# Kernel optimization log

Hardware: AMD Instinct MI355X
Metric: run time of the kernel (lower is better)

Reference implementation:

```python
import jax, jax.numpy as jnp
import numpy as np

# norse default LIF/LI parameters
DT = 0.001
TAU_SYN_INV = 200.0
TAU_MEM_INV = 100.0
V_TH = 1.0
ALPHA = 100.0        # SuperSpike surrogate slope (method='super', alpha=100)
T_ENC = 40           # ConstantCurrentLIFEncoder(40)
SCALE = 50.0

STATE_DIM = 256
ACTIONS = 18
HIDDEN = 128
BATCH = 1024

@jax.custom_vjp
def spike(x):
    return (x > 0).astype(x.dtype)

def _spike_fwd(x):
    return spike(x), x

def _spike_bwd(x, g):
    # SuperSpike surrogate: 1 / (alpha*|x| + 1)^2
    return (g / (ALPHA * jnp.abs(x) + 1.0) ** 2,)

spike.defvjp(_spike_fwd, _spike_bwd)

def encode(current):
    # constant-current LIF encoder: current [B, D] -> spikes [T_ENC, B, D]
    def step(v, _):
        v = v + DT * TAU_MEM_INV * (-v + current)   # v_leak = 0
        z = spike(v - V_TH)
        v = (1.0 - z) * v                            # reset to v_reset = 0
        return v, z
    _, zs = jax.lax.scan(step, jnp.zeros_like(current), None, length=T_ENC)
    return zs

def snn_forward(x, w_in, w_rec, w_actor, w_critic):
    # encode positive and negative rectified currents, concat on feature dim
    xs = jnp.concatenate([encode(jax.nn.relu(SCALE * x)),
                          encode(jax.nn.relu(-SCALE * x))], axis=2)  # [T, B, 2D]
    B = x.shape[0]
    H = w_in.shape[0]
    A = w_actor.shape[0]
    dt_ = x.dtype
    carry0 = (jnp.zeros((B, H), dt_), jnp.zeros((B, H), dt_), jnp.zeros((B, H), dt_),
              jnp.zeros((B, A), dt_), jnp.zeros((B, A), dt_),
              jnp.zeros((B, 1), dt_), jnp.zeros((B, 1), dt_))

    def step(carry, x_t):
        z, v, i, va, ia, vc, ic = carry
        # --- recurrent LIFCell (norse lif_step) ---
        v_dec = v + DT * TAU_MEM_INV * (-v + i)      # dv uses pre-decay i
        i_dec = i - DT * TAU_SYN_INV * i
        z_new = spike(v_dec - V_TH)
        v_new = (1.0 - z_new) * v_dec                # reset by z to v_reset = 0
        i_new = i_dec + x_t @ w_in.T + z @ w_rec.T   # recurrent input uses old z
        # --- LICell actor readout (norse li_step) ---
        va_new = va + DT * TAU_MEM_INV * (-va + ia)
        ia_new = ia - DT * TAU_SYN_INV * ia + z_new @ w_actor.T
        # --- LICell critic readout ---
        vc_new = vc + DT * TAU_MEM_INV * (-vc + ic)
        ic_new = ic - DT * TAU_SYN_INV * ic + z_new @ w_critic.T
        return (z_new, v_new, i_new, va_new, ia_new, vc_new, ic_new), (va_new, vc_new)

    _, (volt_a, volt_c) = jax.lax.scan(step, carry0, xs)
    m_a = jnp.max(volt_a, axis=0)                    # max over time
    m_c = jnp.max(volt_c, axis=0)
    return jax.nn.softmax(m_a, axis=1), m_c


def setup_inputs() -> dict:
    key = jax.random.key(0)
    k0, k1, k2, k3, k4 = jax.random.split(key, 5)
    in_feat = 2 * STATE_DIM
    x = jax.random.normal(k0, (BATCH, STATE_DIM), dtype=jnp.float32)
    # norse init: randn * sqrt(2 / input_size)
    w_in = jax.random.normal(k1, (HIDDEN, in_feat), dtype=jnp.float32) * np.sqrt(2.0 / in_feat)
    w_rec = jax.random.normal(k2, (HIDDEN, HIDDEN), dtype=jnp.float32) * np.sqrt(2.0 / HIDDEN)
    w_actor = jax.random.normal(k3, (ACTIONS, HIDDEN), dtype=jnp.float32) * np.sqrt(2.0 / HIDDEN)
    w_critic = jax.random.normal(k4, (1, HIDDEN), dtype=jnp.float32) * np.sqrt(2.0 / HIDDEN)
    return {"x": x, "w_in": w_in, "w_rec": w_rec, "w_actor": w_actor, "w_critic": w_critic}


def reference(x, w_in, w_rec, w_actor, w_critic):
    return snn_forward(x, w_in, w_rec, w_actor, w_critic)
```

## Files before the change

### kernel.cpp

```cpp
#include <hip/hip_runtime.h>
#include <hip/hip_bf16.h>
#include <stdint.h>

typedef __attribute__((ext_vector_type(4))) float f32x4;
typedef __attribute__((ext_vector_type(8))) short s16x8;
typedef __attribute__((ext_vector_type(4))) unsigned int u32x4;

#define OFF_I 2621440

__device__ __forceinline__ void lut_entry(uint32_t by, uint32_t* r) {
    uint32_t r0 = 0, r1 = 0, r2 = 0, r3 = 0;
    if (by & 1)   r0 |= 0x3F80u;
    if (by & 2)   r0 |= 0x3F800000u;
    if (by & 4)   r1 |= 0x3F80u;
    if (by & 8)   r1 |= 0x3F800000u;
    if (by & 16)  r2 |= 0x3F80u;
    if (by & 32)  r2 |= 0x3F800000u;
    if (by & 64)  r3 |= 0x3F80u;
    if (by & 128) r3 |= 0x3F800000u;
    r[0] = r0; r[1] = r1; r[2] = r2; r[3] = r3;
}

__global__ __launch_bounds__(256) void k_encode(const float* __restrict__ x,
                                                uint32_t* __restrict__ spk) {
    int gid  = blockIdx.x * 256 + threadIdx.x;
    int b    = gid >> 9;
    int f    = gid & 511;
    int lane = threadIdx.x & 63;
    float xv  = x[b * 256 + (f & 255)];
    float cur = (f < 256) ? fmaxf(50.f * xv, 0.f) : fmaxf(-50.f * xv, 0.f);
    int wbase = (f >> 6) << 1;
    float v = 0.f;
    for (int t = 0; t < 40; ++t) {
        v = v + 0.1f * (cur - v);
        bool z = (v - 1.0f) > 0.f;
        unsigned long long m = __ballot(z);
        if (z) v = 0.f;
        if (lane == 0)
            *(unsigned long long*)&spk[(size_t)(t * 1024 + b) * 16 + wbase] = m;
    }
}

__global__ __launch_bounds__(512, 1) void k_ingemm(const uint32_t* __restrict__ spk,
                                                   const float* __restrict__ w_in,
                                                   float* __restrict__ I) {
    __shared__ uint32_t lut[256][4];
    __shared__ float tile[16][128];
    const int tid = threadIdx.x;
    if (tid < 256) lut_entry(tid, lut[tid]);
    const int lane = tid & 63, wid = tid >> 6;
    const int fr = lane & 15, fo = lane >> 4;
    const int n0 = wid * 16;

#define LOADB(i) s16x8 bh##i, bl##i; { \
    const float* p = w_in + (n0 + fr) * 512 + (i) * 32 + fo * 8; \
    f32x4 fa = *(const f32x4*)p; f32x4 fb = *(const f32x4*)(p + 4); \
    _Pragma("unroll") for (int j = 0; j < 8; ++j) { \
        float f = (j < 4) ? fa[j] : fb[j - 4]; \
        __hip_bfloat16 hb = __float2bfloat16(f); \
        float r1 = f - __bfloat162float(hb); \
        __hip_bfloat16 lb = __float2bfloat16(r1); \
        bh##i[j] = (short)*(unsigned short*)&hb; \
        bl##i[j] = (short)*(unsigned short*)&lb; } }
    LOADB(0)  LOADB(1)  LOADB(2)  LOADB(3)  LOADB(4)  LOADB(5)  LOADB(6)  LOADB(7)
    LOADB(8)  LOADB(9)  LOADB(10) LOADB(11) LOADB(12) LOADB(13) LOADB(14) LOADB(15)
#undef LOADB
    asm volatile("" : "+v"(bh0), "+v"(bh1), "+v"(bh2),  "+v"(bh3),
                      "+v"(bh4), "+v"(bh5), "+v"(bh6),  "+v"(bh7),
                      "+v"(bh8), "+v"(bh9), "+v"(bh10), "+v"(bh11),
                      "+v"(bh12),"+v"(bh13),"+v"(bh14), "+v"(bh15));
    asm volatile("" : "+v"(bl0), "+v"(bl1), "+v"(bl2),  "+v"(bl3),
                      "+v"(bl4), "+v"(bl5), "+v"(bl6),  "+v"(bl7),
                      "+v"(bl8), "+v"(bl9), "+v"(bl10), "+v"(bl11),
                      "+v"(bl12),"+v"(bl13),"+v"(bl14), "+v"(bl15));
    __syncthreads();

    const int m0 = blockIdx.x * 160;
    const int srow = tid >> 5;
    const int sc0  = (tid & 31) * 4;
    for (int mt = 0; mt < 10; ++mt) {
        int mrow = m0 + mt * 16 + fr;
        u32x4 w0 = *(const u32x4*)&spk[mrow * 16];
        u32x4 w1 = *(const u32x4*)&spk[mrow * 16 + 4];
        u32x4 w2 = *(const u32x4*)&spk[mrow * 16 + 8];
        u32x4 w3 = *(const u32x4*)&spk[mrow * 16 + 12];
        f32x4 acc = (f32x4)0.f;
#define KSTEP(i, WSEL) { uint32_t by = ((WSEL) >> (fo * 8)) & 0xFFu; \
        union { u32x4 u; s16x8 v; } cv; cv.u = *(const u32x4*)lut[by]; \
        acc = __builtin_amdgcn_mfma_f32_16x16x32_bf16(cv.v, bh##i, acc, 0, 0, 0); \
        acc = __builtin_amdgcn_mfma_f32_16x16x32_bf16(cv.v, bl##i, acc, 0, 0, 0); }
        KSTEP(0,  w0[0]) KSTEP(1,  w0[1]) KSTEP(2,  w0[2]) KSTEP(3,  w0[3])
        KSTEP(4,  w1[0]) KSTEP(5,  w1[1]) KSTEP(6,  w1[2]) KSTEP(7,  w1[3])
        KSTEP(8,  w2[0]) KSTEP(9,  w2[1]) KSTEP(10, w2[2]) KSTEP(11, w2[3])
        KSTEP(12, w3[0]) KSTEP(13, w3[1]) KSTEP(14, w3[2]) KSTEP(15, w3[3])
#undef KSTEP
        __syncthreads();
#pragma unroll
        for (int r = 0; r < 4; ++r)
            tile[fo * 4 + r][n0 + fr] = acc[r];
        __syncthreads();
        f32x4 vv = *(const f32x4*)&tile[srow][sc0];
        *(f32x4*)&I[(size_t)(m0 + mt * 16 + srow) * 128 + sc0] = vv;
    }
}

__global__ __launch_bounds__(512, 1) void k_recur_ro(const float* __restrict__ I,
                                                     const float* __restrict__ w_rec,
                                                     const float* __restrict__ w_actor,
                                                     const float* __restrict__ w_critic,
                                                     float* __restrict__ out) {
    __shared__ uint32_t lut[256][4];
    __shared__ __align__(16) uint16_t zm16[2][16][8];
    __shared__ float smax[16][20];
    const int tid = threadIdx.x;
    if (tid < 256) lut_entry(tid, lut[tid]);
    if (tid < 128) ((uint16_t*)zm16)[tid] = 0;
    const int lane = tid & 63, w = tid >> 6;
    const int fr = lane & 15, fo = lane >> 4;
    const int n0 = w * 16;
    const int b0 = blockIdx.x * 16;

#define LOADW(ks) s16x8 H##ks, L##ks, Q##ks; { \
    const float* p = w_rec + (n0 + fr) * 128 + (ks) * 32 + fo * 8; \
    _Pragma("unroll") for (int j = 0; j < 8; ++j) { \
        float f = p[j]; \
        __hip_bfloat16 hb = __float2bfloat16(f); \
        float r1 = f - __bfloat162float(hb); \
        __hip_bfloat16 lb = __float2bfloat16(r1); \
        float r2 = r1 - __bfloat162float(lb); \
        __hip_bfloat16 qb = __float2bfloat16(r2); \
        H##ks[j] = (short)*(unsigned short*)&hb; \
        L##ks[j] = (short)*(unsigned short*)&lb; \
        Q##ks[j] = (short)*(unsigned short*)&qb; } }
    LOADW(0) LOADW(1) LOADW(2) LOADW(3)
#undef LOADW
    asm volatile("" : "+v"(H0), "+v"(H1), "+v"(H2), "+v"(H3),
                      "+v"(L0), "+v"(L1), "+v"(L2), "+v"(L3),
                      "+v"(Q0), "+v"(Q1), "+v"(Q2), "+v"(Q3));

    s16x8 rbh[4], rbl[4];
    const int a_ch = w * 16 + fr;
    const float* asrc = (w < 2)
        ? ((a_ch < 18) ? (w_actor + a_ch * 128) : ((a_ch == 18) ? w_critic : nullptr))
        : nullptr;
#pragma unroll
    for (int ks = 0; ks < 4; ++ks) {
#pragma unroll
        for (int j = 0; j < 8; ++j) {
            float f = asrc ? asrc[ks * 32 + fo * 8 + j] : 0.f;
            __hip_bfloat16 hb = __float2bfloat16(f);
            float r1 = f - __bfloat162float(hb);
            __hip_bfloat16 lb = __float2bfloat16(r1);
            rbh[ks][j] = (short)*(unsigned short*)&hb;
            rbl[ks][j] = (short)*(unsigned short*)&lb;
        }
    }
    f32x4 rva = (f32x4)0.f, ria = (f32x4)0.f, rma = (f32x4)(-1e30f);

    f32x4 v0 = (f32x4)0.f, c0 = (f32x4)0.f;

#define ILOAD(dst, t_) { _Pragma("unroll") for (int r = 0; r < 4; ++r) \
    dst[r] = I[(size_t)((t_) * 1024 + b0 + fo * 4 + r) * 128 + n0 + fr]; }
    f32x4 icur;
    ILOAD(icur, 0)
    __syncthreads();

    for (int t = 0; t < 40; ++t) {
        int tn = (t < 39) ? t + 1 : 39;
        f32x4 inxt;
        ILOAD(inxt, tn)

        u32x4 zw = *(const u32x4*)zm16[t & 1][fr];
        union { u32x4 u; s16x8 v; } a0, a1, a2, a3;
        a0.u = *(const u32x4*)lut[(zw[0] >> (fo * 8)) & 0xFFu];
        a1.u = *(const u32x4*)lut[(zw[1] >> (fo * 8)) & 0xFFu];
        a2.u = *(const u32x4*)lut[(zw[2] >> (fo * 8)) & 0xFFu];
        a3.u = *(const u32x4*)lut[(zw[3] >> (fo * 8)) & 0xFFu];

        f32x4 r0 = (f32x4)0.f;
#define RECK(ks, av) \
        r0 = __builtin_amdgcn_mfma_f32_16x16x32_bf16(av, H##ks, r0, 0, 0, 0); \
        r0 = __builtin_amdgcn_mfma_f32_16x16x32_bf16(av, L##ks, r0, 0, 0, 0); \
        r0 = __builtin_amdgcn_mfma_f32_16x16x32_bf16(av, Q##ks, r0, 0, 0, 0);
        RECK(0, a0.v) RECK(1, a1.v) RECK(2, a2.v) RECK(3, a3.v)
#undef RECK

        f32x4 vd = v0 + 0.1f * (c0 - v0);
        f32x4 id = c0 - 0.2f * c0;
        unsigned long long B0, B1, B2, B3;
        bool z;
        z = (vd[0] - 1.0f) > 0.f; B0 = __ballot(z); if (z) vd[0] = 0.f;
        z = (vd[1] - 1.0f) > 0.f; B1 = __ballot(z); if (z) vd[1] = 0.f;
        z = (vd[2] - 1.0f) > 0.f; B2 = __ballot(z); if (z) vd[2] = 0.f;
        z = (vd[3] - 1.0f) > 0.f; B3 = __ballot(z); if (z) vd[3] = 0.f;
        v0 = vd;

        if (lane < 16) {
            int m = lane, rq = m & 3, sh = (m >> 2) * 16;
            unsigned long long s = (rq == 0) ? B0 : (rq == 1) ? B1 : (rq == 2) ? B2 : B3;
            zm16[(t & 1) ^ 1][m][w] = (uint16_t)((s >> sh) & 0xFFFFu);
        }

        c0 = (id + icur) + r0;
        icur = inxt;
        __syncthreads();

        if (w < 2) {
            u32x4 zw2 = *(const u32x4*)zm16[(t & 1) ^ 1][fr];
            f32x4 racc = (f32x4)0.f;
#pragma unroll
            for (int ks = 0; ks < 4; ++ks) {
                uint32_t by = (zw2[ks] >> (fo * 8)) & 0xFFu;
                union { u32x4 u; s16x8 v; } cv;
                cv.u = *(const u32x4*)lut[by];
                racc = __builtin_amdgcn_mfma_f32_16x16x32_bf16(cv.v, rbh[ks], racc, 0, 0, 0);
                racc = __builtin_amdgcn_mfma_f32_16x16x32_bf16(cv.v, rbl[ks], racc, 0, 0, 0);
            }
            f32x4 nva = rva + 0.1f * (ria - rva);
            ria = ria - 0.2f * ria + racc;
            rva = nva;
#pragma unroll
            for (int r = 0; r < 4; ++r)
                rma[r] = fmaxf(rma[r], nva[r]);
        }
    }
#undef ILOAD

    if (w == 0) {
#pragma unroll
        for (int r = 0; r < 4; ++r) smax[fo * 4 + r][fr] = rma[r];
    } else if (w == 1 && fr < 3) {
#pragma unroll
        for (int r = 0; r < 4; ++r) smax[fo * 4 + r][16 + fr] = rma[r];
    }
    __syncthreads();
    if (tid < 16) {
        int row = tid;
        float mx = -1e30f;
#pragma unroll
        for (int a2 = 0; a2 < 18; ++a2) mx = fmaxf(mx, smax[row][a2]);
        float s = 0.f;
#pragma unroll
        for (int a2 = 0; a2 < 18; ++a2) s += expf(smax[row][a2] - mx);
#pragma unroll
        for (int a2 = 0; a2 < 18; ++a2)
            out[(b0 + row) * 18 + a2] = expf(smax[row][a2] - mx) / s;
        out[18432 + b0 + row] = smax[row][18];
    }
}

extern "C" void kernel_launch(void* const* d_in, const int* in_sizes, int n_in,
                              void* d_out, int out_size, void* d_ws, size_t ws_size,
                              hipStream_t stream) {
    const float* x        = (const float*)d_in[0];
    const float* w_in     = (const float*)d_in[1];
    const float* w_rec    = (const float*)d_in[2];
    const float* w_actor  = (const float*)d_in[3];
    const float* w_critic = (const float*)d_in[4];
    float* out = (float*)d_out;
    char* ws = (char*)d_ws;
    uint32_t* spk = (uint32_t*)ws;
    float*    I   = (float*)(ws + OFF_I);

    hipLaunchKernelGGL(k_encode,   dim3(2048), dim3(256), 0, stream, x, spk);
    hipLaunchKernelGGL(k_ingemm,   dim3(256),  dim3(512), 0, stream, spk, w_in, I);
    hipLaunchKernelGGL(k_recur_ro, dim3(64),   dim3(512), 0, stream,
                       I, w_rec, w_actor, w_critic, out);
}
```

Baseline: 129.4 us.

## Fuse encoder, input GEMM and recurrence into a single per-batch-tile kernel

Merges the three kernels into one launch of 64 blocks. Each block encodes its own 16 batch rows into shared-memory spike bitmasks and computes the input projection for the next timestep inside the recurrent loop, overlapping it with the recurrence. This removes the global round trip for the spike tensor and the large I tensor, plus two kernel launches. Readout weights move from registers to shared memory. The trade-off is that the input GEMM now runs on only 64 blocks instead of 256, adding 32 MFMAs per timestep to the serial recurrent chain. Register pressure is also high, since the w_in and w_rec fragments are both held in registers.

After: 135.7 us. +4.9%, slower.

```diff
diff --git a/kernel.cpp b/kernel.cpp
--- a/kernel.cpp
+++ b/kernel.cpp
@@ -5,8 +5,6 @@
 typedef __attribute__((ext_vector_type(4))) float f32x4;
 typedef __attribute__((ext_vector_type(8))) short s16x8;
 typedef __attribute__((ext_vector_type(4))) unsigned int u32x4;
-
-#define OFF_I 2621440
 
 __device__ __forceinline__ void lut_entry(uint32_t by, uint32_t* r) {
     uint32_t r0 = 0, r1 = 0, r2 = 0, r3 = 0;
@@ -21,36 +19,59 @@
     r[0] = r0; r[1] = r1; r[2] = r2; r[3] = r3;
 }
 
-__global__ __launch_bounds__(256) void k_encode(const float* __restrict__ x,
-                                                uint32_t* __restrict__ spk) {
-    int gid  = blockIdx.x * 256 + threadIdx.x;
-    int b    = gid >> 9;
-    int f    = gid & 511;
-    int lane = threadIdx.x & 63;
-    float xv  = x[b * 256 + (f & 255)];
-    float cur = (f < 256) ? fmaxf(50.f * xv, 0.f) : fmaxf(-50.f * xv, 0.f);
-    int wbase = (f >> 6) << 1;
-    float v = 0.f;
-    for (int t = 0; t < 40; ++t) {
-        v = v + 0.1f * (cur - v);
-        bool z = (v - 1.0f) > 0.f;
-        unsigned long long m = __ballot(z);
-        if (z) v = 0.f;
-        if (lane == 0)
-            *(unsigned long long*)&spk[(size_t)(t * 1024 + b) * 16 + wbase] = m;
-    }
-}
-
-__global__ __launch_bounds__(512, 1) void k_ingemm(const uint32_t* __restrict__ spk,
-                                                   const float* __restrict__ w_in,
-                                                   float* __restrict__ I) {
+__global__ __launch_bounds__(512, 1) void k_all(const float* __restrict__ x,
+                                                const float* __restrict__ w_in,
+                                                const float* __restrict__ w_rec,
+                                                const float* __restrict__ w_actor,
+                                                const float* __restrict__ w_critic,
+                                                float* __restrict__ out) {
     __shared__ uint32_t lut[256][4];
-    __shared__ float tile[16][128];
+    __shared__ uint32_t spkL[40][16][20];
+    __shared__ __hip_bfloat16 rbh[32][136];
+    __shared__ __hip_bfloat16 rbl[32][136];
+    __shared__ __align__(16) uint16_t zm16[2][16][8];
+    __shared__ float smax[16][20];
+
     const int tid = threadIdx.x;
+    const int lane = tid & 63, w = tid >> 6;
+    const int fr = lane & 15, fo = lane >> 4;
+    const int n0 = w * 16;
+    const int b0 = blockIdx.x * 16;
+
     if (tid < 256) lut_entry(tid, lut[tid]);
-    const int lane = tid & 63, wid = tid >> 6;
-    const int fr = lane & 15, fo = lane >> 4;
-    const int n0 = wid * 16;
+    if (tid < 128) ((uint16_t*)zm16)[tid] = 0;
+
+    for (int idx = tid; idx < 32 * 128; idx += 512) {
+        int a = idx >> 7, k = idx & 127;
+        float f = (a < 18) ? w_actor[a * 128 + k] : ((a == 18) ? w_critic[k] : 0.f);
+        __hip_bfloat16 hb = __float2bfloat16(f);
+        rbh[a][k] = hb;
+        rbl[a][k] = __float2bfloat16(f - __bfloat162float(hb));
+    }
+
+    {
+        const int er = tid >> 5, eh = tid & 31;
+        const float* xp = x + (size_t)(b0 + er) * 256 + (eh & 15) * 16;
+        const float sgn = (eh < 16) ? 50.f : -50.f;
+        float cur0,cur1,cur2,cur3,cur4,cur5,cur6,cur7,cur8,cur9,curA,curB,curC,curD,curE,curF;
+        float4 x4;
+        x4 = *(const float4*)(xp + 0);  cur0 = fmaxf(sgn*x4.x,0.f); cur1 = fmaxf(sgn*x4.y,0.f); cur2 = fmaxf(sgn*x4.z,0.f); cur3 = fmaxf(sgn*x4.w,0.f);
+        x4 = *(const float4*)(xp + 4);  cur4 = fmaxf(sgn*x4.x,0.f); cur5 = fmaxf(sgn*x4.y,0.f); cur6 = fmaxf(sgn*x4.z,0.f); cur7 = fmaxf(sgn*x4.w,0.f);
+        x4 = *(const float4*)(xp + 8);  cur8 = fmaxf(sgn*x4.x,0.f); cur9 = fmaxf(sgn*x4.y,0.f); curA = fmaxf(sgn*x4.z,0.f); curB = fmaxf(sgn*x4.w,0.f);
+        x4 = *(const float4*)(xp + 12); curC = fmaxf(sgn*x4.x,0.f); curD = fmaxf(sgn*x4.y,0.f); curE = fmaxf(sgn*x4.z,0.f); curF = fmaxf(sgn*x4.w,0.f);
+        float v0_=0,v1_=0,v2_=0,v3_=0,v4_=0,v5_=0,v6_=0,v7_=0,v8_=0,v9_=0,vA_=0,vB_=0,vC_=0,vD_=0,vE_=0,vF_=0;
+        for (int t = 0; t < 40; ++t) {
+            uint32_t bits = 0;
+#define ENC(V, C, J) { V = V + 0.1f * (C - V); bool z = (V - 1.0f) > 0.f; \
+                       if (z) { bits |= (1u << (J)); V = 0.f; } }
+            ENC(v0_,cur0,0) ENC(v1_,cur1,1) ENC(v2_,cur2,2) ENC(v3_,cur3,3)
+            ENC(v4_,cur4,4) ENC(v5_,cur5,5) ENC(v6_,cur6,6) ENC(v7_,cur7,7)
+            ENC(v8_,cur8,8) ENC(v9_,cur9,9) ENC(vA_,curA,10) ENC(vB_,curB,11)
+            ENC(vC_,curC,12) ENC(vD_,curD,13) ENC(vE_,curE,14) ENC(vF_,curF,15)
+#undef ENC
+            ((uint16_t*)&spkL[t][er][0])[eh] = (uint16_t)bits;
+        }
+    }
 
 #define LOADB(i) s16x8 bh##i, bl##i; { \
     const float* p = w_in + (n0 + fr) * 512 + (i) * 32 + fo * 8; \
@@ -73,52 +94,6 @@
                       "+v"(bl4), "+v"(bl5), "+v"(bl6),  "+v"(bl7),
                       "+v"(bl8), "+v"(bl9), "+v"(bl10), "+v"(bl11),
                       "+v"(bl12),"+v"(bl13),"+v"(bl14), "+v"(bl15));
-    __syncthreads();
-
-    const int m0 = blockIdx.x * 160;
-    const int srow = tid >> 5;
-    const int sc0  = (tid & 31) * 4;
-    for (int mt = 0; mt < 10; ++mt) {
-        int mrow = m0 + mt * 16 + fr;
-        u32x4 w0 = *(const u32x4*)&spk[mrow * 16];
-        u32x4 w1 = *(const u32x4*)&spk[mrow * 16 + 4];
-        u32x4 w2 = *(const u32x4*)&spk[mrow * 16 + 8];
-        u32x4 w3 = *(const u32x4*)&spk[mrow * 16 + 12];
-        f32x4 acc = (f32x4)0.f;
-#define KSTEP(i, WSEL) { uint32_t by = ((WSEL) >> (fo * 8)) & 0xFFu; \
-        union { u32x4 u; s16x8 v; } cv; cv.u = *(const u32x4*)lut[by]; \
-        acc = __builtin_amdgcn_mfma_f32_16x16x32_bf16(cv.v, bh##i, acc, 0, 0, 0); \
-        acc = __builtin_amdgcn_mfma_f32_16x16x32_bf16(cv.v, bl##i, acc, 0, 0, 0); }
-        KSTEP(0,  w0[0]) KSTEP(1,  w0[1]) KSTEP(2,  w0[2]) KSTEP(3,  w0[3])
-        KSTEP(4,  w1[0]) KSTEP(5,  w1[1]) KSTEP(6,  w1[2]) KSTEP(7,  w1[3])
-        KSTEP(8,  w2[0]) KSTEP(9,  w2[1]) KSTEP(10, w2[2]) KSTEP(11, w2[3])
-        KSTEP(12, w3[0]) KSTEP(13, w3[1]) KSTEP(14, w3[2]) KSTEP(15, w3[3])
-#undef KSTEP
-        __syncthreads();
-#pragma unroll
-        for (int r = 0; r < 4; ++r)
-            tile[fo * 4 + r][n0 + fr] = acc[r];
-        __syncthreads();
-        f32x4 vv = *(const f32x4*)&tile[srow][sc0];
-        *(f32x4*)&I[(size_t)(m0 + mt * 16 + srow) * 128 + sc0] = vv;
-    }
-}
-
-__global__ __launch_bounds__(512, 1) void k_recur_ro(const float* __restrict__ I,
-                                                     const float* __restrict__ w_rec,
-                                                     const float* __restrict__ w_actor,
-                                                     const float* __restrict__ w_critic,
-                                                     float* __restrict__ out) {
-    __shared__ uint32_t lut[256][4];
-    __shared__ __align__(16) uint16_t zm16[2][16][8];
-    __shared__ float smax[16][20];
-    const int tid = threadIdx.x;
-    if (tid < 256) lut_entry(tid, lut[tid]);
-    if (tid < 128) ((uint16_t*)zm16)[tid] = 0;
-    const int lane = tid & 63, w = tid >> 6;
-    const int fr = lane & 15, fo = lane >> 4;
-    const int n0 = w * 16;
-    const int b0 = blockIdx.x * 16;
 
 #define LOADW(ks) s16x8 H##ks, L##ks, Q##ks; { \
     const float* p = w_rec + (n0 + fr) * 128 + (ks) * 32 + fo * 8; \
@@ -138,37 +113,50 @@
                       "+v"(L0), "+v"(L1), "+v"(L2), "+v"(L3),
                       "+v"(Q0), "+v"(Q1), "+v"(Q2), "+v"(Q3));
 
-    s16x8 rbh[4], rbl[4];
-    const int a_ch = w * 16 + fr;
-    const float* asrc = (w < 2)
-        ? ((a_ch < 18) ? (w_actor + a_ch * 128) : ((a_ch == 18) ? w_critic : nullptr))
-        : nullptr;
-#pragma unroll
-    for (int ks = 0; ks < 4; ++ks) {
-#pragma unroll
-        for (int j = 0; j < 8; ++j) {
-            float f = asrc ? asrc[ks * 32 + fo * 8 + j] : 0.f;
-            __hip_bfloat16 hb = __float2bfloat16(f);
-            float r1 = f - __bfloat162float(hb);
-            __hip_bfloat16 lb = __float2bfloat16(r1);
-            rbh[ks][j] = (short)*(unsigned short*)&hb;
-            rbl[ks][j] = (short)*(unsigned short*)&lb;
-        }
-    }
+    __syncthreads();
+
+#define ICHAIN(dst, T_) { \
+        u32x4 s0 = *(const u32x4*)&spkL[T_][fr][0]; \
+        u32x4 s1 = *(const u32x4*)&spkL[T_][fr][4]; \
+        u32x4 s2 = *(const u32x4*)&spkL[T_][fr][8]; \
+        u32x4 s3 = *(const u32x4*)&spkL[T_][fr][12]; \
+        f32x4 acc = (f32x4)0.f; \
+        union { u32x4 u; s16x8 v; } cv; \
+        uint32_t by; \
+        _Pragma("unroll") for (int ks = 0; ks < 16; ++ks) { \
+            uint32_t word = (ks < 4) ? s0[ks & 3] : (ks < 8) ? s1[ks & 3] \
+                          : (ks < 12) ? s2[ks & 3] : s3[ks & 3]; \
+            by = (word >> (fo * 8)) & 0xFFu; \
+            cv.u = *(const u32x4*)lut[by]; \
+            switch (ks) { \
+            case 0:  acc = __builtin_amdgcn_mfma_f32_16x16x32_bf16(cv.v, bh0,  acc,0,0,0); acc = __builtin_amdgcn_mfma_f32_16x16x32_bf16(cv.v, bl0,  acc,0,0,0); break; \
+            case 1:  acc = __builtin_amdgcn_mfma_f32_16x16x32_bf16(cv.v, bh1,  acc,0,0,0); acc = __builtin_amdgcn_mfma_f32_16x16x32_bf16(cv.v, bl1,  acc,0,0,0); break; \
+            case 2:  acc = __builtin_amdgcn_mfma_f32_16x16x32_bf16(cv.v, bh2,  acc,0,0,0); acc = __builtin_amdgcn_mfma_f32_16x16x32_bf16(cv.v, bl2,  acc,0,0,0); break; \
+            case 3:  acc = __builtin_amdgcn_mfma_f32_16x16x32_bf16(cv.v, bh3,  acc,0,0,0); acc = __builtin_amdgcn_mfma_f32_16x16x32_bf16(cv.v, bl3,  acc,0,0,0); break; \
+            case 4:  acc = __builtin_amdgcn_mfma_f32_16x16x32_bf16(cv.v, bh4,  acc,0,0,0); acc = __builtin_amdgcn_mfma_f32_16x16x32_bf16(cv.v, bl4,  acc,0,0,0); break; \
+            case 5:  acc = __builtin_amdgcn_mfma_f32_16x16x32_bf16(cv.v, bh5,  acc,0,0,0); acc = __builtin_amdgcn_mfma_f32_16x16x32_bf16(cv.v, bl5,  acc,0,0,0); break; \
+            case 6:  acc = __builtin_amdgcn_mfma_f32_16x16x32_bf16(cv.v, bh6,  acc,0,0,0); acc = __builtin_amdgcn_mfma_f32_16x16x32_bf16(cv.v, bl6,  acc,0,0,0); break; \
+            case 7:  acc = __builtin_amdgcn_mfma_f32_16x16x32_bf16(cv.v, bh7,  acc,0,0,0); acc = __builtin_amdgcn_mfma_f32_16x16x32_bf16(cv.v, bl7,  acc,0,0,0); break; \
+            case 8:  acc = __builtin_amdgcn_mfma_f32_16x16x32_bf16(cv.v, bh8,  acc,0,0,0); acc = __builtin_amdgcn_mfma_f32_16x16x32_bf16(cv.v, bl8,  acc,0,0,0); break; \
+            case 9:  acc = __builtin_amdgcn_mfma_f32_16x16x32_bf16(cv.v, bh9,  acc,0,0,0); acc = __builtin_amdgcn_mfma_f32_16x16x32_bf16(cv.v, bl9,  acc,0,0,0); break; \
+            case 10: acc = __builtin_amdgcn_mfma_f32_16x16x32_bf16(cv.v, bh10, acc,0,0,0); acc = __builtin_amdgcn_mfma_f32_16x16x32_bf16(cv.v, bl10, acc,0,0,0); break; \
+            case 11: acc = __builtin_amdgcn_mfma_f32_16x16x32_bf16(cv.v, bh11, acc,0,0,0); acc = __builtin_amdgcn_mfma_f32_16x16x32_bf16(cv.v, bl11, acc,0,0,0); break; \
+            case 12: acc = __builtin_amdgcn_mfma_f32_16x16x32_bf16(cv.v, bh12, acc,0,0,0); acc = __builtin_amdgcn_mfma_f32_16x16x32_bf16(cv.v, bl12, acc,0,0,0); break; \
+            case 13: acc = __builtin_amdgcn_mfma_f32_16x16x32_bf16(cv.v, bh13, acc,0,0,0); acc = __builtin_amdgcn_mfma_f32_16x16x32_bf16(cv.v, bl13, acc,0,0,0); break; \
+            case 14: acc = __builtin_amdgcn_mfma_f32_16x16x32_bf16(cv.v, bh14, acc,0,0,0); acc = __builtin_amdgcn_mfma_f32_16x16x32_bf16(cv.v, bl14, acc,0,0,0); break; \
+            default: acc = __builtin_amdgcn_mfma_f32_16x16x32_bf16(cv.v, bh15, acc,0,0,0); acc = __builtin_amdgcn_mfma_f32_16x16x32_bf16(cv.v, bl15, acc,0,0,0); break; \
+            } \
+        } \
+        dst = acc; }
+
+    f32x4 Icur;
+    ICHAIN(Icur, 0)
+
+    f32x4 v0 = (f32x4)0.f, c0 = (f32x4)0.f;
     f32x4 rva = (f32x4)0.f, ria = (f32x4)0.f, rma = (f32x4)(-1e30f);
-
-    f32x4 v0 = (f32x4)0.f, c0 = (f32x4)0.f;
-
-#define ILOAD(dst, t_) { _Pragma("unroll") for (int r = 0; r < 4; ++r) \
-    dst[r] = I[(size_t)((t_) * 1024 + b0 + fo * 4 + r) * 128 + n0 + fr]; }
-    f32x4 icur;
-    ILOAD(icur, 0)
-    __syncthreads();
 
     for (int t = 0; t < 40; ++t) {
         int tn = (t < 39) ? t + 1 : 39;
-        f32x4 inxt;
-        ILOAD(inxt, tn)
 
         u32x4 zw = *(const u32x4*)zm16[t & 1][fr];
         union { u32x4 u; s16x8 v; } a0, a1, a2, a3;
@@ -176,7 +164,6 @@
         a1.u = *(const u32x4*)lut[(zw[1] >> (fo * 8)) & 0xFFu];
         a2.u = *(const u32x4*)lut[(zw[2] >> (fo * 8)) & 0xFFu];
         a3.u = *(const u32x4*)lut[(zw[3] >> (fo * 8)) & 0xFFu];
-
         f32x4 r0 = (f32x4)0.f;
 #define RECK(ks, av) \
         r0 = __builtin_amdgcn_mfma_f32_16x16x32_bf16(av, H##ks, r0, 0, 0, 0); \
@@ -184,6 +171,9 @@
         r0 = __builtin_amdgcn_mfma_f32_16x16x32_bf16(av, Q##ks, r0, 0, 0, 0);
         RECK(0, a0.v) RECK(1, a1.v) RECK(2, a2.v) RECK(3, a3.v)
 #undef RECK
+
+        f32x4 Inxt;
+        ICHAIN(Inxt, tn)
 
         f32x4 vd = v0 + 0.1f * (c0 - v0);
         f32x4 id = c0 - 0.2f * c0;
@@ -201,20 +191,23 @@
             zm16[(t & 1) ^ 1][m][w] = (uint16_t)((s >> sh) & 0xFFFFu);
         }
 
-        c0 = (id + icur) + r0;
-        icur = inxt;
+        c0 = (id + Icur) + r0;
+        Icur = Inxt;
         __syncthreads();
 
         if (w < 2) {
             u32x4 zw2 = *(const u32x4*)zm16[(t & 1) ^ 1][fr];
+            const int a_ch = w * 16 + fr;
             f32x4 racc = (f32x4)0.f;
 #pragma unroll
             for (int ks = 0; ks < 4; ++ks) {
                 uint32_t by = (zw2[ks] >> (fo * 8)) & 0xFFu;
                 union { u32x4 u; s16x8 v; } cv;
                 cv.u = *(const u32x4*)lut[by];
-                racc = __builtin_amdgcn_mfma_f32_16x16x32_bf16(cv.v, rbh[ks], racc, 0, 0, 0);
-                racc = __builtin_amdgcn_mfma_f32_16x16x32_bf16(cv.v, rbl[ks], racc, 0, 0, 0);
+                s16x8 fh = *(const s16x8*)&rbh[a_ch][ks * 32 + fo * 8];
+                s16x8 fl = *(const s16x8*)&rbl[a_ch][ks * 32 + fo * 8];
+                racc = __builtin_amdgcn_mfma_f32_16x16x32_bf16(cv.v, fh, racc, 0, 0, 0);
+                racc = __builtin_amdgcn_mfma_f32_16x16x32_bf16(cv.v, fl, racc, 0, 0, 0);
             }
             f32x4 nva = rva + 0.1f * (ria - rva);
             ria = ria - 0.2f * ria + racc;
@@ -224,7 +217,7 @@
                 rma[r] = fmaxf(rma[r], nva[r]);
         }
     }
-#undef ILOAD
+#undef ICHAIN
 
     if (w == 0) {
 #pragma unroll
@@ -258,12 +251,8 @@
     const float* w_actor  = (const float*)d_in[3];
     const float* w_critic = (const float*)d_in[4];
     float* out = (float*)d_out;
-    char* ws = (char*)d_ws;
-    uint32_t* spk = (uint32_t*)ws;
-    float*    I   = (float*)(ws + OFF_I);
-
-    hipLaunchKernelGGL(k_encode,   dim3(2048), dim3(256), 0, stream, x, spk);
-    hipLaunchKernelGGL(k_ingemm,   dim3(256),  dim3(512), 0, stream, spk, w_in, I);
-    hipLaunchKernelGGL(k_recur_ro, dim3(64),   dim3(512), 0, stream,
-                       I, w_rec, w_actor, w_critic, out);
+    (void)d_ws; (void)ws_size;
+
+    hipLaunchKernelGGL(k_all, dim3(64), dim3(512), 0, stream,
+                       x, w_in, w_rec, w_actor, w_critic, out);
 }
```
